# Kernel tuning notes

Hardware: AMD Instinct MI355X
Metric: run time of the kernel (lower is better)

The kernel has to match this reference:

```python
import jax, jax.numpy as jnp
import numpy as np

N_NODES = 100000
N_FEAT = 128
N_EDGES = 1600000


def setup_inputs() -> dict:
    key = jax.random.key(0)
    k1, k2, k3 = jax.random.split(key, 3)
    x = jax.random.normal(k1, (N_NODES, N_FEAT), dtype=jnp.float32)
    edge_index = jax.random.randint(k2, (2, N_EDGES), 0, N_NODES, dtype=jnp.int32)
    edge_weight = jax.random.uniform(k3, (N_EDGES,), dtype=jnp.float32)
    return {"x": x, "edge_index": edge_index, "edge_weight": edge_weight}


def reference(x, edge_index, edge_weight):
    # output[i] = (1/deg_i) * sum_{j in N(i) u {i}} w_ij * x[j]
    n = x.shape[0]
    src, dst = edge_index[0], edge_index[1]
    # add self-loops with weight 1
    loop = jnp.arange(n, dtype=src.dtype)
    src = jnp.concatenate([src, loop])
    dst = jnp.concatenate([dst, loop])
    w = jnp.concatenate([edge_weight, jnp.ones((n,), dtype=edge_weight.dtype)])
    # row-degree normalization: degree over src (row index of adjacency)
    deg = jax.ops.segment_sum(w, src, num_segments=n)
    deg = jnp.maximum(deg, 1.0)  # clamp(min=1.0)
    w = w / deg[src]
    # sparse adj @ x  ==  scatter-add of scaled gathered rows
    msg = w[:, None] * x[dst]            # (E+N, F)
    out = jax.ops.segment_sum(msg, src, num_segments=n)  # (N, F)
    return out
```

## Files before the change

### kernel.cpp

```cpp
#include <hip/hip_runtime.h>
#include <hip/hip_fp16.h>

#define N_NODES 100000
#define N_FEAT  128
#define N_EDGES 1600000
#define OVF_CAP 65536

constexpr size_t align_up(size_t x) { return (x + 255) & ~size_t(255); }

#define NBUCK   1563
#define BCAP    1280
#define CHUNK   8192
#define NBLK_A  ((N_EDGES + CHUNK - 1) / CHUNK)
#define CONVBLK 2048
#define NCONV   (N_NODES * N_FEAT / 4)
#define NXH     (N_NODES * 64)

constexpr size_t P_GCUR = 0;
constexpr size_t P_DEGX = P_GCUR + align_up(NBUCK * 4);
constexpr size_t P_OVFC = P_DEGX + align_up(N_NODES * 4);
constexpr size_t P_INV  = P_OVFC + 256;
constexpr size_t P_OVF  = P_INV  + align_up(N_NODES * 4);
constexpr size_t P_XH   = P_OVF  + align_up(OVF_CAP * 12);
constexpr size_t P_BKT  = P_XH   + align_up((size_t)NXH * 4);
constexpr size_t WS_P   = P_BKT  + (size_t)NBUCK * BCAP * 8;
constexpr size_t P_ZERO = P_OVFC + 256;

__global__ __launch_bounds__(256) void k_part_conv(
    const int* __restrict__ src, const int* __restrict__ dst,
    const float* __restrict__ w, const float* __restrict__ x,
    uint2* __restrict__ xh_u2,
    int* __restrict__ gcur, unsigned long long* __restrict__ bucket,
    float* __restrict__ degx, int* __restrict__ ovf_cnt, int* __restrict__ ovf) {
    int tid = threadIdx.x;
    if (blockIdx.x >= NBLK_A) {
        const float4* x4 = (const float4*)x;
        int stride = (gridDim.x - NBLK_A) * 256;
        for (int g = (blockIdx.x - NBLK_A) * 256 + tid; g < NCONV; g += stride) {
            float4 v = x4[g];
            __half2 h0 = __floats2half2_rn(v.x, v.y);
            __half2 h1 = __floats2half2_rn(v.z, v.w);
            uint2 u;
            __builtin_memcpy(&u.x, &h0, 4);
            __builtin_memcpy(&u.y, &h1, 4);
            xh_u2[g] = u;
        }
        return;
    }
    __shared__ int hist[NBUCK];
    __shared__ int cbase[NBUCK];
    int e0 = blockIdx.x * CHUNK;
    int e1 = min(e0 + CHUNK, N_EDGES);

    for (int i = tid; i < NBUCK; i += 256) hist[i] = 0;
    __syncthreads();
    for (int e = e0 + tid; e < e1; e += 256)
        atomicAdd(&hist[src[e] >> 6], 1);
    __syncthreads();
    for (int i = tid; i < NBUCK; i += 256) {
        int c = hist[i];
        cbase[i] = c ? atomicAdd(&gcur[i], c) : 0;
        hist[i] = 0;
    }
    __syncthreads();
    for (int e = e0 + tid; e < e1; e += 256) {
        int   s  = src[e];
        int   d  = dst[e];
        float ww = w[e];
        int k  = s >> 6;
        int ln = s & 63;
        int pos = cbase[k] + atomicAdd(&hist[k], 1);
        if (pos < BCAP) {
            unsigned hi = ((unsigned)ln << 17) | (unsigned)d;
            unsigned long long pk = ((unsigned long long)hi << 32) | __float_as_uint(ww);
            bucket[(size_t)k * BCAP + pos] = pk;
        } else {
            atomicAdd(&degx[s], ww);
            int o = atomicAdd(ovf_cnt, 1);
            if (o < OVF_CAP) { ovf[o*3] = s; ovf[o*3+1] = d; ovf[o*3+2] = __float_as_int(ww); }
        }
    }
}

__global__ __launch_bounds__(512) void k_bagg(
    const int* __restrict__ gcur, const unsigned long long* __restrict__ bucket,
    const unsigned* __restrict__ xh_u, const float* __restrict__ degx,
    float* __restrict__ inv_arr, float2* __restrict__ out2) {
    __shared__ uint2 sbuf[BCAP];
    __shared__ int hist[64];
    __shared__ int rowo[64];
    __shared__ int curo[64];

    int bk   = blockIdx.x;
    int tid  = threadIdx.x;
    int lane = tid & 63;
    int wv   = tid >> 6;
    int n0   = bk * 64;
    int cnt  = min(gcur[bk], BCAP);

    if (tid < 64) { hist[tid] = 0; curo[tid] = 0; }
    __syncthreads();

    for (int i = tid; i < cnt; i += 512) {
        unsigned hi = (unsigned)(bucket[(size_t)bk * BCAP + i] >> 32);
        atomicAdd(&hist[(hi >> 17) & 63], 1);
    }
    __syncthreads();

    if (tid < 64) {
        int v = hist[tid];
        int sc = v;
        #pragma unroll
        for (int off = 1; off < 64; off <<= 1) {
            int t = __shfl_up(sc, off);
            if (lane >= off) sc += t;
        }
        rowo[tid] = sc - v;
    }
    __syncthreads();

    for (int i = tid; i < cnt; i += 512) {
        unsigned long long ev = bucket[(size_t)bk * BCAP + i];
        uint2 e; e.x = (unsigned)ev; e.y = (unsigned)(ev >> 32);
        int ln = (e.y >> 17) & 63;
        int pos = rowo[ln] + atomicAdd(&curo[ln], 1);
        sbuf[pos] = e;
    }
    __syncthreads();

    for (int i = 0; i < 8; ++i) {
        int n    = wv * 8 + i;
        int node = n0 + n;
        if (node >= N_NODES) break;
        int c = hist[n];
        int r = rowo[n];

        unsigned us = xh_u[(size_t)node * 64 + lane];
        __half2 hs; __builtin_memcpy(&hs, &us, 4);
        float2 acc = __half22float2(hs);
        float wlane = 0.0f;

        for (int base = 0; base < c; base += 64) {
            int idx = base + lane;
            uint2 e = make_uint2(0u, 0u);
            if (idx < c) e = sbuf[r + idx];
            float ew = __uint_as_float(e.x);
            int   ed = (int)(e.y & 0x1FFFFu);
            wlane += ew;
            int m = min(64, c - base);
            int j = 0;
            for (; j + 7 < m; j += 8) {
                float ww[8]; float2 vv[8];
                #pragma unroll
                for (int q = 0; q < 8; ++q) {
                    float w8 = __shfl(ew, j + q);
                    int   d8 = __shfl(ed, j + q);
                    unsigned u = xh_u[(size_t)d8 * 64 + lane];
                    __half2 h; __builtin_memcpy(&h, &u, 4);
                    vv[q] = __half22float2(h);
                    ww[q] = w8;
                }
                #pragma unroll
                for (int q = 0; q < 8; ++q) { acc.x += ww[q]*vv[q].x; acc.y += ww[q]*vv[q].y; }
            }
            for (; j < m; ++j) {
                float w1 = __shfl(ew, j);
                int   d1 = __shfl(ed, j);
                unsigned u = xh_u[(size_t)d1 * 64 + lane];
                __half2 h; __builtin_memcpy(&h, &u, 4);
                float2 v = __half22float2(h);
                acc.x += w1 * v.x; acc.y += w1 * v.y;
            }
        }
        float ws = wlane;
        #pragma unroll
        for (int off = 1; off < 64; off <<= 1) ws += __shfl_xor(ws, off);
        float deg = 1.0f + ws + degx[node];
        float inv = 1.0f / fmaxf(deg, 1.0f);
        if (lane == 0) inv_arr[node] = inv;
        out2[(size_t)node * 64 + lane] = make_float2(acc.x * inv, acc.y * inv);
    }
}

__global__ void k_ovf(const int* __restrict__ ovf_cnt, const int* __restrict__ ovf,
                      const float* __restrict__ inv_arr,
                      const float* __restrict__ x, float* __restrict__ out) {
    int n = min(*ovf_cnt, OVF_CAP);
    for (int i = blockIdx.x * blockDim.x + threadIdx.x; i < n;
         i += gridDim.x * blockDim.x) {
        int s = ovf[i*3], d = ovf[i*3+1];
        float sc = __int_as_float(ovf[i*3+2]) * inv_arr[s];
        for (int f = 0; f < N_FEAT; ++f)
            atomicAdd(&out[(size_t)s * N_FEAT + f], sc * x[(size_t)d * N_FEAT + f]);
    }
}

#define SLOTS_F 64
constexpr size_t G_CUR  = 0;
constexpr size_t G_DEGX = G_CUR  + align_up(N_NODES * 4);
constexpr size_t G_OVFC = G_DEGX + align_up(N_NODES * 4);
constexpr size_t G_INV  = G_OVFC + 256;
constexpr size_t G_OVF  = G_INV  + align_up(N_NODES * 4);
constexpr size_t G_SLOT = G_OVF  + align_up(OVF_CAP * 12);
constexpr size_t WS_G   = G_SLOT + (size_t)N_NODES * SLOTS_F * 8;
constexpr size_t G_ZERO = G_OVFC + 256;

__global__ void g_build(const int* __restrict__ src, const int* __restrict__ dst,
                        const float* __restrict__ w,
                        int* __restrict__ cursor, uint2* __restrict__ slots,
                        float* __restrict__ degx,
                        int* __restrict__ ovf_cnt, int* __restrict__ ovf) {
    int e = blockIdx.x * blockDim.x + threadIdx.x;
    if (e >= N_EDGES) return;
    int s = src[e], d = dst[e];
    float ww = w[e];
    int c = atomicAdd(&cursor[s], 1);
    if (c < SLOTS_F) {
        uint2 v; v.x = (unsigned)d; v.y = __float_as_uint(ww);
        slots[(size_t)s * SLOTS_F + c] = v;
    } else {
        atomicAdd(&degx[s], ww);
        int o = atomicAdd(ovf_cnt, 1);
        if (o < OVF_CAP) { ovf[o*3] = s; ovf[o*3+1] = d; ovf[o*3+2] = __float_as_int(ww); }
    }
}

__global__ __launch_bounds__(256) void g_agg(
    const int* __restrict__ cursor, const uint2* __restrict__ slots,
    const float* __restrict__ degx, float* __restrict__ inv_arr,
    const float2* __restrict__ x2, float2* __restrict__ out2) {
    int wid  = (int)((blockIdx.x * (long long)blockDim.x + threadIdx.x) >> 6);
    int lane = threadIdx.x & 63;
    if (wid >= N_NODES) return;
    int c = min(cursor[wid], SLOTS_F);
    int dv = 0; float wv = 0.0f;
    if (lane < c) {
        uint2 sl = slots[(size_t)wid * SLOTS_F + lane];
        dv = (int)sl.x; wv = __uint_as_float(sl.y);
    }
    float wsum = wv;
    #pragma unroll
    for (int off = 1; off < 64; off <<= 1) wsum += __shfl_xor(wsum, off);
    float deg = 1.0f + wsum + degx[wid];
    float inv = 1.0f / fmaxf(deg, 1.0f);
    if (lane == 0) inv_arr[wid] = inv;
    float2 acc = x2[(size_t)wid * 64 + lane];
    int k = 0;
    for (; k + 3 < c; k += 4) {
        int   d0 = __shfl(dv, k),   d1 = __shfl(dv, k+1);
        int   d2 = __shfl(dv, k+2), d3 = __shfl(dv, k+3);
        float w0 = __shfl(wv, k),   w1 = __shfl(wv, k+1);
        float w2 = __shfl(wv, k+2), w3 = __shfl(wv, k+3);
        float2 v0 = x2[(size_t)d0 * 64 + lane];
        float2 v1 = x2[(size_t)d1 * 64 + lane];
        float2 v2 = x2[(size_t)d2 * 64 + lane];
        float2 v3 = x2[(size_t)d3 * 64 + lane];
        acc.x += w0*v0.x + w1*v1.x + w2*v2.x + w3*v3.x;
        acc.y += w0*v0.y + w1*v1.y + w2*v2.y + w3*v3.y;
    }
    for (; k < c; ++k) {
        int d = __shfl(dv, k); float w = __shfl(wv, k);
        float2 v = x2[(size_t)d * 64 + lane];
        acc.x += w * v.x; acc.y += w * v.y;
    }
    out2[(size_t)wid * 64 + lane] = make_float2(acc.x * inv, acc.y * inv);
}

constexpr size_t F_CNT = 0;
constexpr size_t F_ROW = F_CNT + align_up(N_NODES * 4);
constexpr size_t F_CUR = F_ROW + align_up(N_NODES * 4);
constexpr size_t F_DEG = F_CUR + align_up(N_NODES * 4);
constexpr size_t F_TOT = F_DEG + align_up(N_NODES * 4);
constexpr size_t F_DST = F_TOT + 256;
constexpr size_t F_W   = F_DST + align_up(N_EDGES * 4);
constexpr size_t WS_CSR = F_W + N_EDGES * 4;

__global__ void c_init(int* cnt, float* deg, int* total) {
    int i = blockIdx.x * blockDim.x + threadIdx.x;
    if (i < N_NODES) { cnt[i] = 0; deg[i] = 1.0f; }
    if (i == 0) *total = 0;
}
__global__ void c_count(const int* src, const float* w, int* cnt, float* deg) {
    int e = blockIdx.x * blockDim.x + threadIdx.x;
    if (e < N_EDGES) { int s = src[e]; atomicAdd(&cnt[s], 1); atomicAdd(&deg[s], w[e]); }
}
__global__ void c_alloc(const int* cnt, int* rowstart, int* cursor, float* deg, int* total) {
    int i = blockIdx.x * blockDim.x + threadIdx.x;
    if (i < N_NODES) {
        int c = cnt[i]; int s = atomicAdd(total, c);
        rowstart[i] = s; cursor[i] = s;
        deg[i] = 1.0f / fmaxf(deg[i], 1.0f);
    }
}
__global__ void c_scatter(const int* src, const int* dst, const float* w,
                          int* cursor, int* csr_dst, float* csr_w) {
    int e = blockIdx.x * blockDim.x + threadIdx.x;
    if (e < N_EDGES) {
        int pos = atomicAdd(&cursor[src[e]], 1);
        csr_dst[pos] = dst[e]; csr_w[pos] = w[e];
    }
}
__global__ __launch_bounds__(256) void c_agg(
    const int* rowstart, const int* cnt, const float* inv,
    const int* csr_dst, const float* csr_w,
    const float2* x2, float2* out2) {
    int wid  = (int)((blockIdx.x * (long long)blockDim.x + threadIdx.x) >> 6);
    int lane = threadIdx.x & 63;
    if (wid >= N_NODES) return;
    int s = rowstart[wid], c = cnt[wid];
    float2 acc = x2[(size_t)wid * 64 + lane];
    for (int base = 0; base < c; base += 64) {
        int dv = 0; float wv = 0.0f;
        int idx = base + lane;
        if (idx < c) { dv = csr_dst[s + idx]; wv = csr_w[s + idx]; }
        int m = min(64, c - base);
        for (int k = 0; k < m; ++k) {
            int d = __shfl(dv, k); float w = __shfl(wv, k);
            float2 v = x2[(size_t)d * 64 + lane];
            acc.x += w * v.x; acc.y += w * v.y;
        }
    }
    float si = inv[wid];
    out2[(size_t)wid * 64 + lane] = make_float2(acc.x * si, acc.y * si);
}

__global__ void fb_init_deg(float* deg) {
    int i = blockIdx.x * blockDim.x + threadIdx.x;
    if (i < N_NODES) deg[i] = 1.0f;
}
__global__ void fb_accum_deg(const int* src, const float* w, float* deg) {
    int e = blockIdx.x * blockDim.x + threadIdx.x;
    if (e < N_EDGES) atomicAdd(&deg[src[e]], w[e]);
}
__global__ void fb_inv_deg(float* deg) {
    int i = blockIdx.x * blockDim.x + threadIdx.x;
    if (i < N_NODES) deg[i] = 1.0f / fmaxf(deg[i], 1.0f);
}
__global__ void fb_self(const float4* x4, const float* inv, float4* out4) {
    int idx = blockIdx.x * blockDim.x + threadIdx.x;
    if (idx < N_NODES * (N_FEAT / 4)) {
        int node = idx >> 5; float s = inv[node];
        float4 v = x4[idx];
        out4[idx] = make_float4(v.x*s, v.y*s, v.z*s, v.w*s);
    }
}
__global__ void fb_edges(const int* src, const int* dst, const float* w,
                         const float* inv, const float4* x4, float* out) {
    long long gid = (long long)blockIdx.x * blockDim.x + threadIdx.x;
    int e = (int)(gid >> 5); int lane = (int)(gid & 31);
    if (e < N_EDGES) {
        int s = src[e];
        float sc = w[e] * inv[s];
        float4 v = x4[(long long)dst[e] * (N_FEAT/4) + lane];
        float* ob = out + (long long)s * N_FEAT + lane * 4;
        atomicAdd(ob+0, sc*v.x); atomicAdd(ob+1, sc*v.y);
        atomicAdd(ob+2, sc*v.z); atomicAdd(ob+3, sc*v.w);
    }
}

extern "C" void kernel_launch(void* const* d_in, const int* in_sizes, int n_in,
                              void* d_out, int out_size, void* d_ws, size_t ws_size,
                              hipStream_t stream) {
    const float* x          = (const float*)d_in[0];
    const int*   edge_index = (const int*)d_in[1];
    const float* edge_w     = (const float*)d_in[2];
    const int* src = edge_index;
    const int* dst = edge_index + N_EDGES;
    float* out = (float*)d_out;
    const int B = 256;

    if (ws_size >= WS_P) {
        char* ws = (char*)d_ws;
        int*      gcur    = (int*)     (ws + P_GCUR);
        float*    degx    = (float*)   (ws + P_DEGX);
        int*      ovf_cnt = (int*)     (ws + P_OVFC);
        float*    inv_arr = (float*)   (ws + P_INV);
        int*      ovf     = (int*)     (ws + P_OVF);
        uint2*    xh_u2   = (uint2*)   (ws + P_XH);
        unsigned* xh_u    = (unsigned*)(ws + P_XH);
        unsigned long long* bucket = (unsigned long long*)(ws + P_BKT);

        hipMemsetAsync(d_ws, 0, P_ZERO, stream);
        k_part_conv<<<NBLK_A + CONVBLK, 256, 0, stream>>>(
            src, dst, edge_w, x, xh_u2, gcur, bucket, degx, ovf_cnt, ovf);
        k_bagg<<<NBUCK, 512, 0, stream>>>(
            gcur, bucket, xh_u, degx, inv_arr, (float2*)out);
        k_ovf<<<32, 256, 0, stream>>>(ovf_cnt, ovf, inv_arr, x, out);
        return;
    }

    if (ws_size >= WS_G) {
        char* ws = (char*)d_ws;
        int*   cursor  = (int*)  (ws + G_CUR);
        float* degx    = (float*)(ws + G_DEGX);
        int*   ovf_cnt = (int*)  (ws + G_OVFC);
        float* inv_arr = (float*)(ws + G_INV);
        int*   ovf     = (int*)  (ws + G_OVF);
        uint2* slots   = (uint2*)(ws + G_SLOT);
        hipMemsetAsync(d_ws, 0, G_ZERO, stream);
        g_build<<<(N_EDGES + B - 1) / B, B, 0, stream>>>(
            src, dst, edge_w, cursor, slots, degx, ovf_cnt, ovf);
        long long t_agg = (long long)N_NODES * 64;
        g_agg<<<(int)((t_agg + B - 1) / B), B, 0, stream>>>(
            cursor, slots, degx, inv_arr, (const float2*)x, (float2*)out);
        k_ovf<<<32, 256, 0, stream>>>(ovf_cnt, ovf, inv_arr, x, out);
        return;
    }

    if (ws_size >= WS_CSR) {
        char* ws = (char*)d_ws;
        int*   cnt      = (int*)  (ws + F_CNT);
        int*   rowstart = (int*)  (ws + F_ROW);
        int*   cursor   = (int*)  (ws + F_CUR);
        float* deg      = (float*)(ws + F_DEG);
        int*   total    = (int*)  (ws + F_TOT);
        int*   csr_dst  = (int*)  (ws + F_DST);
        float* csr_w    = (float*)(ws + F_W);
        c_init<<<(N_NODES + B - 1) / B, B, 0, stream>>>(cnt, deg, total);
        c_count<<<(N_EDGES + B - 1) / B, B, 0, stream>>>(src, edge_w, cnt, deg);
        c_alloc<<<(N_NODES + B - 1) / B, B, 0, stream>>>(cnt, rowstart, cursor, deg, total);
        c_scatter<<<(N_EDGES + B - 1) / B, B, 0, stream>>>(src, dst, edge_w, cursor,
                                                           csr_dst, csr_w);
        long long t_agg = (long long)N_NODES * 64;
        c_agg<<<(int)((t_agg + B - 1) / B), B, 0, stream>>>(
            rowstart, cnt, deg, csr_dst, csr_w, (const float2*)x, (float2*)out);
        return;
    }

    float* deg = (float*)d_ws;
    fb_init_deg<<<(N_NODES + B - 1) / B, B, 0, stream>>>(deg);
    fb_accum_deg<<<(N_EDGES + B - 1) / B, B, 0, stream>>>(src, edge_w, deg);
    fb_inv_deg<<<(N_NODES + B - 1) / B, B, 0, stream>>>(deg);
    int n4 = N_NODES * (N_FEAT / 4);
    fb_self<<<(n4 + B - 1) / B, B, 0, stream>>>((const float4*)x, deg, (float4*)out);
    long long total = (long long)N_EDGES * 32;
    fb_edges<<<(int)((total + B - 1) / B), B, 0, stream>>>(
        src, dst, edge_w, deg, (const float4*)x, out);
}
```

Before: 123.8 us.

## Split each wave into half-waves gathering two edges at once with 8-byte loads

The aggregation kernel now has each 64-lane wave handle two edges per step: each half-wave of 32 lanes loads one full fp16 row with 8-byte loads instead of the whole wave loading 4 bytes per lane. Edge records are read straight from shared memory instead of through cross-lane shuffles, and the halves are combined with one xor-shuffle at the end. Bucket entries are also loaded into registers once and reused for both the histogram and the scatter passes, instead of being read from global memory twice. This aims to raise memory-level parallelism and cut shuffle and instruction overhead, at the cost of a final cross-half reduction and half the lanes sitting idle on the store.

```diff
diff --git a/kernel.cpp b/kernel.cpp
--- a/kernel.cpp
+++ b/kernel.cpp
@@ -84,8 +84,8 @@
 
 __global__ __launch_bounds__(512) void k_bagg(
     const int* __restrict__ gcur, const unsigned long long* __restrict__ bucket,
-    const unsigned* __restrict__ xh_u, const float* __restrict__ degx,
-    float* __restrict__ inv_arr, float2* __restrict__ out2) {
+    const uint2* __restrict__ xh2, const float* __restrict__ degx,
+    float* __restrict__ inv_arr, float4* __restrict__ out4) {
     __shared__ uint2 sbuf[BCAP];
     __shared__ int hist[64];
     __shared__ int rowo[64];
@@ -95,16 +95,24 @@
     int tid  = threadIdx.x;
     int lane = tid & 63;
     int wv   = tid >> 6;
+    int h    = lane >> 5;
+    int il   = lane & 31;
     int n0   = bk * 64;
     int cnt  = min(gcur[bk], BCAP);
 
     if (tid < 64) { hist[tid] = 0; curo[tid] = 0; }
     __syncthreads();
 
-    for (int i = tid; i < cnt; i += 512) {
-        unsigned hi = (unsigned)(bucket[(size_t)bk * BCAP + i] >> 32);
-        atomicAdd(&hist[(hi >> 17) & 63], 1);
-    }
+    uint2 er0 = make_uint2(0u, 0u), er1 = er0, er2 = er0;
+    {
+        const uint2* bsrc = (const uint2*)(bucket + (size_t)bk * BCAP);
+        if (tid < cnt)        er0 = bsrc[tid];
+        if (tid + 512 < cnt)  er1 = bsrc[tid + 512];
+        if (tid + 1024 < cnt) er2 = bsrc[tid + 1024];
+    }
+    if (tid < cnt)        atomicAdd(&hist[(er0.y >> 17) & 63], 1);
+    if (tid + 512 < cnt)  atomicAdd(&hist[(er1.y >> 17) & 63], 1);
+    if (tid + 1024 < cnt) atomicAdd(&hist[(er2.y >> 17) & 63], 1);
     __syncthreads();
 
     if (tid < 64) {
@@ -119,12 +127,17 @@
     }
     __syncthreads();
 
-    for (int i = tid; i < cnt; i += 512) {
-        unsigned long long ev = bucket[(size_t)bk * BCAP + i];
-        uint2 e; e.x = (unsigned)ev; e.y = (unsigned)(ev >> 32);
-        int ln = (e.y >> 17) & 63;
-        int pos = rowo[ln] + atomicAdd(&curo[ln], 1);
-        sbuf[pos] = e;
+    if (tid < cnt) {
+        int ln = (er0.y >> 17) & 63;
+        sbuf[rowo[ln] + atomicAdd(&curo[ln], 1)] = er0;
+    }
+    if (tid + 512 < cnt) {
+        int ln = (er1.y >> 17) & 63;
+        sbuf[rowo[ln] + atomicAdd(&curo[ln], 1)] = er1;
+    }
+    if (tid + 1024 < cnt) {
+        int ln = (er2.y >> 17) & 63;
+        sbuf[rowo[ln] + atomicAdd(&curo[ln], 1)] = er2;
     }
     __syncthreads();
 
@@ -135,50 +148,54 @@
         int c = hist[n];
         int r = rowo[n];
 
-        unsigned us = xh_u[(size_t)node * 64 + lane];
-        __half2 hs; __builtin_memcpy(&hs, &us, 4);
-        float2 acc = __half22float2(hs);
-        float wlane = 0.0f;
-
-        for (int base = 0; base < c; base += 64) {
-            int idx = base + lane;
-            uint2 e = make_uint2(0u, 0u);
-            if (idx < c) e = sbuf[r + idx];
-            float ew = __uint_as_float(e.x);
-            int   ed = (int)(e.y & 0x1FFFFu);
-            wlane += ew;
-            int m = min(64, c - base);
-            int j = 0;
-            for (; j + 7 < m; j += 8) {
-                float ww[8]; float2 vv[8];
-                #pragma unroll
-                for (int q = 0; q < 8; ++q) {
-                    float w8 = __shfl(ew, j + q);
-                    int   d8 = __shfl(ed, j + q);
-                    unsigned u = xh_u[(size_t)d8 * 64 + lane];
-                    __half2 h; __builtin_memcpy(&h, &u, 4);
-                    vv[q] = __half22float2(h);
-                    ww[q] = w8;
-                }
-                #pragma unroll
-                for (int q = 0; q < 8; ++q) { acc.x += ww[q]*vv[q].x; acc.y += ww[q]*vv[q].y; }
+        float4 acc = make_float4(0.f, 0.f, 0.f, 0.f);
+        if (h == 0) {
+            uint2 u = xh2[(size_t)node * 32 + il];
+            __half2 ha, hb;
+            __builtin_memcpy(&ha, &u.x, 4);
+            __builtin_memcpy(&hb, &u.y, 4);
+            float2 va = __half22float2(ha), vb = __half22float2(hb);
+            acc = make_float4(va.x, va.y, vb.x, vb.y);
+        }
+        float wdeg = 0.0f;
+
+        for (int j = 0; j < c; j += 8) {
+            float ews[4]; uint2 vs[4];
+            #pragma unroll
+            for (int p = 0; p < 4; ++p) {
+                int idx = j + 2 * p + h;
+                bool ok = idx < c;
+                uint2 e = sbuf[r + (ok ? idx : 0)];
+                ews[p] = ok ? __uint_as_float(e.x) : 0.0f;
+                int ed = (int)(e.y & 0x1FFFFu);
+                vs[p] = xh2[(size_t)ed * 32 + il];
             }
-            for (; j < m; ++j) {
-                float w1 = __shfl(ew, j);
-                int   d1 = __shfl(ed, j);
-                unsigned u = xh_u[(size_t)d1 * 64 + lane];
-                __half2 h; __builtin_memcpy(&h, &u, 4);
-                float2 v = __half22float2(h);
-                acc.x += w1 * v.x; acc.y += w1 * v.y;
+            #pragma unroll
+            for (int p = 0; p < 4; ++p) {
+                __half2 ha, hb;
+                __builtin_memcpy(&ha, &vs[p].x, 4);
+                __builtin_memcpy(&hb, &vs[p].y, 4);
+                float2 va = __half22float2(ha), vb = __half22float2(hb);
+                float ew = ews[p];
+                acc.x += ew * va.x; acc.y += ew * va.y;
+                acc.z += ew * vb.x; acc.w += ew * vb.y;
+                if (il == 0) wdeg += ew;
             }
         }
-        float ws = wlane;
+        acc.x += __shfl_xor(acc.x, 32);
+        acc.y += __shfl_xor(acc.y, 32);
+        acc.z += __shfl_xor(acc.z, 32);
+        acc.w += __shfl_xor(acc.w, 32);
+        float ws = wdeg;
         #pragma unroll
         for (int off = 1; off < 64; off <<= 1) ws += __shfl_xor(ws, off);
+
         float deg = 1.0f + ws + degx[node];
         float inv = 1.0f / fmaxf(deg, 1.0f);
         if (lane == 0) inv_arr[node] = inv;
-        out2[(size_t)node * 64 + lane] = make_float2(acc.x * inv, acc.y * inv);
+        if (h == 0)
+            out4[(size_t)node * 32 + il] =
+                make_float4(acc.x * inv, acc.y * inv, acc.z * inv, acc.w * inv);
     }
 }
 
@@ -377,14 +394,13 @@
         float*    inv_arr = (float*)   (ws + P_INV);
         int*      ovf     = (int*)     (ws + P_OVF);
         uint2*    xh_u2   = (uint2*)   (ws + P_XH);
-        unsigned* xh_u    = (unsigned*)(ws + P_XH);
         unsigned long long* bucket = (unsigned long long*)(ws + P_BKT);
 
         hipMemsetAsync(d_ws, 0, P_ZERO, stream);
         k_part_conv<<<NBLK_A + CONVBLK, 256, 0, stream>>>(
             src, dst, edge_w, x, xh_u2, gcur, bucket, degx, ovf_cnt, ovf);
         k_bagg<<<NBUCK, 512, 0, stream>>>(
-            gcur, bucket, xh_u, degx, inv_arr, (float2*)out);
+            gcur, bucket, xh_u2, degx, inv_arr, (float4*)out);
         k_ovf<<<32, 256, 0, stream>>>(ovf_cnt, ovf, inv_arr, x, out);
         return;
     }
```

Measured after the change: 113.9 us. 8.0% less time.
